# Kernel optimization log

Hardware: AMD Instinct MI355X
Metric: run time of the kernel (lower is better)

The kernel has to match this reference:

```python
import jax, jax.numpy as jnp
import numpy as np
from jax import lax

WINDOW_SIZE = 11
SIGMA = 1.5
MAX_VAL = 1.0
C1 = (0.01 * MAX_VAL) ** 2
C2 = (0.03 * MAX_VAL) ** 2
PAD = (WINDOW_SIZE - 1) // 2


def _gaussian_kernel2d(ksize: int, sigma: float) -> jnp.ndarray:
    x = jnp.arange(ksize, dtype=jnp.float32) - ksize // 2
    g = jnp.exp(-(x ** 2) / (2.0 * sigma ** 2))
    g = g / jnp.sum(g)
    return jnp.outer(g, g)  # [k, k]


def _filter2d(x: jnp.ndarray, kernel2d: jnp.ndarray) -> jnp.ndarray:
    # depthwise conv: x [B,C,H,W], kernel repeated per channel -> [C,1,k,k]
    c = x.shape[1]
    k = jnp.broadcast_to(kernel2d[None, None], (c, 1, WINDOW_SIZE, WINDOW_SIZE)).astype(x.dtype)
    return lax.conv_general_dilated(
        x, k,
        window_strides=(1, 1),
        padding=((PAD, PAD), (PAD, PAD)),
        dimension_numbers=("NCHW", "OIHW", "NCHW"),
        feature_group_count=c,
    )


def setup_inputs() -> dict:
    key = jax.random.key(0)
    k1, k2 = jax.random.split(key)
    img1 = jax.random.uniform(k1, (16, 3, 512, 512), dtype=jnp.float32)
    img2 = jax.random.uniform(k2, (16, 3, 512, 512), dtype=jnp.float32)
    return {"img1": img1, "img2": img2}


def reference(img1, img2):
    kernel = _gaussian_kernel2d(WINDOW_SIZE, SIGMA)
    mu1 = _filter2d(img1, kernel)
    mu2 = _filter2d(img2, kernel)
    mu1_sq = mu1 * mu1
    mu2_sq = mu2 * mu2
    mu1_mu2 = mu1 * mu2
    sigma1_sq = _filter2d(img1 * img1, kernel) - mu1_sq
    sigma2_sq = _filter2d(img2 * img2, kernel) - mu2_sq
    sigma12 = _filter2d(img1 * img2, kernel) - mu1_mu2
    ssim_map = ((2.0 * mu1_mu2 + C1) * (2.0 * sigma12 + C2)) / (
        (mu1_sq + mu2_sq + C1) * (sigma1_sq + sigma2_sq + C2)
    )
    loss = jnp.clip(1.0 - ssim_map, 0.0, 1.0) / 2.0
    return jnp.mean(loss)  # reduction='mean'
```

## Files before the change

kernel.cpp:

```cpp
#include <hip/hip_runtime.h>


#define BATCH  16
#define CHAN   3
#define H_     512
#define W_     512
#define HW     (H_ * W_)
#define CH_H   32
#define NSTEP  (CH_H + 10)
#define NPIX   ((long)BATCH*CHAN*H_*W_)

#define GW0 0.0010284f
#define GW1 0.0075988f
#define GW2 0.0360008f
#define GW3 0.1093554f
#define GW4 0.2130056f
#define GW5 0.2660117f

typedef float v2  __attribute__((ext_vector_type(2)));
typedef float v4f __attribute__((ext_vector_type(4)));

__device__ __forceinline__ float wg(int k) {
    return (k == 0 || k == 10) ? GW0
         : (k == 1 || k == 9)  ? GW1
         : (k == 2 || k == 8)  ? GW2
         : (k == 3 || k == 7)  ? GW3
         : (k == 4 || k == 6)  ? GW4 : GW5;
}

__device__ __forceinline__ v2 pfma(v2 a, v2 b, v2 c) {
#if __has_builtin(__builtin_elementwise_fma)
    return __builtin_elementwise_fma(a, b, c);
#else
    v2 r; r.x = fmaf(a.x, b.x, c.x); r.y = fmaf(a.y, b.y, c.y); return r;
#endif
}
__device__ __forceinline__ v2 psfma(float s, v2 b, v2 c) {
    v2 sv; sv.x = s; sv.y = s;
    return pfma(sv, b, c);
}

__device__ __forceinline__ float ssim_retire(float mu1, float mu2,
                                             float x11, float x22, float x12) {
    const float c1 = 1.0e-4f;
    const float c2 = 9.0e-4f;
    float mu1s = mu1 * mu1;
    float mu2s = mu2 * mu2;
    float m12  = mu1 * mu2;
    float num  = (2.0f * m12 + c1) * (2.0f * (x12 - m12) + c2);
    float den  = (mu1s + mu2s + c1) * ((x11 - mu1s) + (x22 - mu2s) + c2);
#if __has_builtin(__builtin_amdgcn_rcpf)
    float l = 1.0f - num * __builtin_amdgcn_rcpf(den);
#else
    float l = 1.0f - num / den;
#endif
    return fminf(fmaxf(l, 0.0f), 1.0f);
}

#define DECL(i) v2 PA##i = {0.f,0.f}, QA##i = {0.f,0.f}, PB##i = {0.f,0.f}, \
                   QB##i = {0.f,0.f}; float EA##i = 0.f, EB##i = 0.f
#define ACCI(i) do { const float wj_ = wg(10 - (i));             \
    PA##i = psfma(wj_, hmmA, PA##i);                             \
    QA##i = psfma(wj_, hssA, QA##i);                             \
    EA##i = fmaf(wj_, hm12A, EA##i);                             \
    PB##i = psfma(wj_, hmmB, PB##i);                             \
    QB##i = psfma(wj_, hssB, QB##i);                             \
    EB##i = fmaf(wj_, hm12B, EB##i); } while (0)
#define SHIFT(i, j) PA##i = PA##j; QA##i = QA##j; EA##i = EA##j; \
                    PB##i = PB##j; QB##i = QB##j; EB##i = EB##j

#define HT_A(ab_, k_) { v2 t = (ab_) * wg(k_); hmmA += t; \
    hssA = pfma(t, (ab_), hssA); hm12A = fmaf(t.x, (ab_).y, hm12A); }
#define HT_B(ab_, k_) { v2 t = (ab_) * wg(k_); hmmB += t; \
    hssB = pfma(t, (ab_), hssB); hm12B = fmaf(t.x, (ab_).y, hm12B); }

__global__ __launch_bounds__(256) void ssim_kernel(const float* __restrict__ img1,
                                                   const float* __restrict__ img2,
                                                   float* __restrict__ out) {
    __shared__ __align__(16) v2 sp[4][144];
    __shared__ float wsum[4];

    const int tid  = threadIdx.x;
    const int lane = tid & 63;
    const int wv   = tid >> 6;

    const int wid   = blockIdx.x * 4 + wv;
    const int plane = wid >> 6;
    const int rem   = wid & 63;
    const int strip = rem & 3;
    const int chunk = rem >> 2;
    const int y0 = chunk * CH_H;
    const int c0 = strip * 128;

    const int  cg   = c0 - 6 + 2 * lane;
    const bool cok  = (cg >= 0);
    const int  cix  = cok ? cg : 0;
    const float msk = cok ? 1.0f : 0.0f;
    const int  hg   = c0 + 122 + 2 * lane;
    const bool hok  = (lane < 6) && (hg + 1 < W_);
    const int  hix  = hok ? hg : 0;
    const float hmsk = hok ? 1.0f : 0.0f;

    const size_t pb = (size_t)plane * HW;
    const float* __restrict__ p1 = img1 + pb;
    const float* __restrict__ p2 = img2 + pb;

    v2* st = sp[wv];

    DECL(0); DECL(1); DECL(2); DECL(3); DECL(4); DECL(5);
    DECL(6); DECL(7); DECL(8); DECL(9); DECL(10);
    float lsum = 0.0f;

    v2 ma, mb, ha, hb;
    {
        int r = y0 - 5;
        bool rok = (unsigned)r < (unsigned)H_;
        size_t off = (size_t)(rok ? r : 0) * W_;
        float mm = rok ? msk : 0.0f, hm = rok ? hmsk : 0.0f;
        ma = *(const v2*)(p1 + off + cix) * mm;
        mb = *(const v2*)(p2 + off + cix) * mm;
        ha = *(const v2*)(p1 + off + hix) * hm;
        hb = *(const v2*)(p2 + off + hix) * hm;
    }

#pragma unroll 2
    for (int step = 0; step < NSTEP; ++step) {
        const int yy = step - 10;

        {
            v4f w; w.x = ma.x; w.y = mb.x; w.z = ma.y; w.w = mb.y;
            *(v4f*)&st[2 * lane] = w;
            if (lane < 6) {
                v4f wh; wh.x = ha.x; wh.y = hb.x; wh.z = ha.y; wh.w = hb.y;
                *(v4f*)&st[128 + 2 * lane] = wh;
            }
        }
        __asm__ __volatile__("" ::: "memory");

        {
            int r = y0 + step - 4;
            bool rok = (unsigned)r < (unsigned)H_;
            size_t off = (size_t)(rok ? r : 0) * W_;
            float mm = rok ? msk : 0.0f, hm = rok ? hmsk : 0.0f;
            ma = *(const v2*)(p1 + off + cix) * mm;
            mb = *(const v2*)(p2 + off + cix) * mm;
            ha = *(const v2*)(p1 + off + hix) * hm;
            hb = *(const v2*)(p2 + off + hix) * hm;
        }

        v2 m1  = st[2 * lane + 1];
        v4f r1 = *(const v4f*)&st[2 * lane + 2];
        v4f r2 = *(const v4f*)&st[2 * lane + 4];
        v4f r3 = *(const v4f*)&st[2 * lane + 6];
        v4f r4 = *(const v4f*)&st[2 * lane + 8];
        v4f r5 = *(const v4f*)&st[2 * lane + 10];
        v2 m12 = st[2 * lane + 12];
        v2 m2  = {r1.x, r1.y}, m3  = {r1.z, r1.w};
        v2 m4  = {r2.x, r2.y}, m5  = {r2.z, r2.w};
        v2 m6  = {r3.x, r3.y}, m7  = {r3.z, r3.w};
        v2 m8  = {r4.x, r4.y}, m9  = {r4.z, r4.w};
        v2 m10 = {r5.x, r5.y}, m11 = {r5.z, r5.w};

        v2 hmmA = m1 * wg(0);
        v2 hssA = hmmA * m1;
        float hm12A = hmmA.x * m1.y;
        HT_A(m2, 1); HT_A(m3, 2); HT_A(m4, 3); HT_A(m5, 4); HT_A(m6, 5);
        HT_A(m7, 6); HT_A(m8, 7); HT_A(m9, 8); HT_A(m10, 9); HT_A(m11, 10);
        v2 hmmB = m2 * wg(0);
        v2 hssB = hmmB * m2;
        float hm12B = hmmB.x * m2.y;
        HT_B(m3, 1); HT_B(m4, 2); HT_B(m5, 3); HT_B(m6, 4); HT_B(m7, 5);
        HT_B(m8, 6); HT_B(m9, 7); HT_B(m10, 8); HT_B(m11, 9); HT_B(m12, 10);
        __asm__ __volatile__("" ::: "memory");

        ACCI(0); ACCI(1); ACCI(2); ACCI(3); ACCI(4); ACCI(5);
        ACCI(6); ACCI(7); ACCI(8); ACCI(9); ACCI(10);

        if (yy >= 0) {
            lsum += ssim_retire(PA0.x, PA0.y, QA0.x, QA0.y, EA0);
            lsum += ssim_retire(PB0.x, PB0.y, QB0.x, QB0.y, EB0);
        }

        SHIFT(0, 1); SHIFT(1, 2); SHIFT(2, 3); SHIFT(3, 4); SHIFT(4, 5);
        SHIFT(5, 6); SHIFT(6, 7); SHIFT(7, 8); SHIFT(8, 9); SHIFT(9, 10);
        PA10 = (v2){0.f, 0.f}; QA10 = (v2){0.f, 0.f}; EA10 = 0.f;
        PB10 = (v2){0.f, 0.f}; QB10 = (v2){0.f, 0.f}; EB10 = 0.f;
    }

#pragma unroll
    for (int off = 32; off > 0; off >>= 1) lsum += __shfl_down(lsum, off);
    if (lane == 0) wsum[wv] = lsum;
    __syncthreads();
    if (tid == 0) {
        float bs = wsum[0] + wsum[1] + wsum[2] + wsum[3];
        atomicAdd(out, bs * (0.5f / (float)NPIX));
    }
}

extern "C" void kernel_launch(void* const* d_in, const int* in_sizes, int n_in,
                              void* d_out, int out_size, void* d_ws, size_t ws_size,
                              hipStream_t stream) {
    const float* img1 = (const float*)d_in[0];
    const float* img2 = (const float*)d_in[1];
    float* out = (float*)d_out;

    hipMemsetAsync(out, 0, sizeof(float), stream);

    ssim_kernel<<<dim3(4 * 16 * BATCH * CHAN / 4), 256, 0, stream>>>(img1, img2, out);
}
```

Measured before the change: 157.0 us.

## Split wave into two half-strips, double chunk height, trim vertical accumulator

Each 64-lane wavefront now covers two 64-column half-strips, one per 32-lane half, with separate shared staging, and row chunks grow from 32 to 64 rows. This shrinks the 10-row vertical halo overhead per output row. The vertical ring drops one register slot by seeding the newest slot directly from the horizontal sums, and blocks are one wave each with a direct atomic per wave. The trade-off is more horizontal halo columns per output (12 per 64 instead of 12 per 128), fewer blocks (1536 waves), and more atomics.

```diff
diff --git a/kernel.cpp b/kernel.cpp
--- a/kernel.cpp
+++ b/kernel.cpp
@@ -6,7 +6,7 @@
 #define H_     512
 #define W_     512
 #define HW     (H_ * W_)
-#define CH_H   32
+#define CH_H   64
 #define NSTEP  (CH_H + 10)
 #define NPIX   ((long)BATCH*CHAN*H_*W_)
 
@@ -74,30 +74,40 @@
 #define HT_B(ab_, k_) { v2 t = (ab_) * wg(k_); hmmB += t; \
     hssB = pfma(t, (ab_), hssB); hm12B = fmaf(t.x, (ab_).y, hm12B); }
 
-__global__ __launch_bounds__(256) void ssim_kernel(const float* __restrict__ img1,
-                                                   const float* __restrict__ img2,
-                                                   float* __restrict__ out) {
-    __shared__ __align__(16) v2 sp[4][144];
-    __shared__ float wsum[4];
+#define LOADROW(r_) do {                                           \
+    int rr_ = (r_);                                                \
+    bool rok_ = (unsigned)rr_ < (unsigned)H_;                      \
+    size_t off_ = ((size_t)(rok_ ? rr_ : 0) << 9);                 \
+    float mm_ = rok_ ? msk  : 0.0f;                                \
+    float hm_ = rok_ ? hmsk : 0.0f;                                \
+    ma = *(const v2*)(p1 + off_ + cix) * mm_;                      \
+    mb = *(const v2*)(p2 + off_ + cix) * mm_;                      \
+    ha = *(const v2*)(p1 + off_ + hix) * hm_;                      \
+    hb = *(const v2*)(p2 + off_ + hix) * hm_; } while (0)
 
-    const int tid  = threadIdx.x;
-    const int lane = tid & 63;
-    const int wv   = tid >> 6;
+__global__ __launch_bounds__(64) void ssim_kernel(const float* __restrict__ img1,
+                                                  const float* __restrict__ img2,
+                                                  float* __restrict__ out) {
+    __shared__ __align__(16) v2 sp[2][80];
 
-    const int wid   = blockIdx.x * 4 + wv;
-    const int plane = wid >> 6;
-    const int rem   = wid & 63;
-    const int strip = rem & 3;
+    const int lane = threadIdx.x & 63;
+    const int half = lane >> 5;
+    const int l    = lane & 31;
+
+    const int wid   = blockIdx.x;
+    const int plane = wid >> 5;
+    const int rem   = wid & 31;
+    const int t     = rem & 3;
     const int chunk = rem >> 2;
-    const int y0 = chunk * CH_H;
-    const int c0 = strip * 128;
+    const int y0  = chunk * CH_H;
+    const int c0h = t * 128 + half * 64;
 
-    const int  cg   = c0 - 6 + 2 * lane;
+    const int  cg   = c0h - 6 + 2 * l;
     const bool cok  = (cg >= 0);
     const int  cix  = cok ? cg : 0;
     const float msk = cok ? 1.0f : 0.0f;
-    const int  hg   = c0 + 122 + 2 * lane;
-    const bool hok  = (lane < 6) && (hg + 1 < W_);
+    const int  hg   = c0h + 58 + 2 * l;
+    const bool hok  = (l < 6) && (hg + 1 < W_);
     const int  hix  = hok ? hg : 0;
     const float hmsk = hok ? 1.0f : 0.0f;
 
@@ -105,23 +115,14 @@
     const float* __restrict__ p1 = img1 + pb;
     const float* __restrict__ p2 = img2 + pb;
 
-    v2* st = sp[wv];
+    v2* st = sp[half];
 
-    DECL(0); DECL(1); DECL(2); DECL(3); DECL(4); DECL(5);
-    DECL(6); DECL(7); DECL(8); DECL(9); DECL(10);
+    DECL(0); DECL(1); DECL(2); DECL(3); DECL(4);
+    DECL(5); DECL(6); DECL(7); DECL(8); DECL(9);
     float lsum = 0.0f;
 
     v2 ma, mb, ha, hb;
-    {
-        int r = y0 - 5;
-        bool rok = (unsigned)r < (unsigned)H_;
-        size_t off = (size_t)(rok ? r : 0) * W_;
-        float mm = rok ? msk : 0.0f, hm = rok ? hmsk : 0.0f;
-        ma = *(const v2*)(p1 + off + cix) * mm;
-        mb = *(const v2*)(p2 + off + cix) * mm;
-        ha = *(const v2*)(p1 + off + hix) * hm;
-        hb = *(const v2*)(p2 + off + hix) * hm;
-    }
+    LOADROW(y0 - 5);
 
 #pragma unroll 2
     for (int step = 0; step < NSTEP; ++step) {
@@ -129,32 +130,23 @@
 
         {
             v4f w; w.x = ma.x; w.y = mb.x; w.z = ma.y; w.w = mb.y;
-            *(v4f*)&st[2 * lane] = w;
-            if (lane < 6) {
+            *(v4f*)&st[2 * l] = w;
+            if (l < 6) {
                 v4f wh; wh.x = ha.x; wh.y = hb.x; wh.z = ha.y; wh.w = hb.y;
-                *(v4f*)&st[128 + 2 * lane] = wh;
+                *(v4f*)&st[64 + 2 * l] = wh;
             }
         }
         __asm__ __volatile__("" ::: "memory");
 
-        {
-            int r = y0 + step - 4;
-            bool rok = (unsigned)r < (unsigned)H_;
-            size_t off = (size_t)(rok ? r : 0) * W_;
-            float mm = rok ? msk : 0.0f, hm = rok ? hmsk : 0.0f;
-            ma = *(const v2*)(p1 + off + cix) * mm;
-            mb = *(const v2*)(p2 + off + cix) * mm;
-            ha = *(const v2*)(p1 + off + hix) * hm;
-            hb = *(const v2*)(p2 + off + hix) * hm;
-        }
+        LOADROW(y0 + step - 4);
 
-        v2 m1  = st[2 * lane + 1];
-        v4f r1 = *(const v4f*)&st[2 * lane + 2];
-        v4f r2 = *(const v4f*)&st[2 * lane + 4];
-        v4f r3 = *(const v4f*)&st[2 * lane + 6];
-        v4f r4 = *(const v4f*)&st[2 * lane + 8];
-        v4f r5 = *(const v4f*)&st[2 * lane + 10];
-        v2 m12 = st[2 * lane + 12];
+        v2 m1  = st[2 * l + 1];
+        v4f r1 = *(const v4f*)&st[2 * l + 2];
+        v4f r2 = *(const v4f*)&st[2 * l + 4];
+        v4f r3 = *(const v4f*)&st[2 * l + 6];
+        v4f r4 = *(const v4f*)&st[2 * l + 8];
+        v4f r5 = *(const v4f*)&st[2 * l + 10];
+        v2 m12 = st[2 * l + 12];
         v2 m2  = {r1.x, r1.y}, m3  = {r1.z, r1.w};
         v2 m4  = {r2.x, r2.y}, m5  = {r2.z, r2.w};
         v2 m6  = {r3.x, r3.y}, m7  = {r3.z, r3.w};
@@ -173,8 +165,8 @@
         HT_B(m8, 6); HT_B(m9, 7); HT_B(m10, 8); HT_B(m11, 9); HT_B(m12, 10);
         __asm__ __volatile__("" ::: "memory");
 
-        ACCI(0); ACCI(1); ACCI(2); ACCI(3); ACCI(4); ACCI(5);
-        ACCI(6); ACCI(7); ACCI(8); ACCI(9); ACCI(10);
+        ACCI(0); ACCI(1); ACCI(2); ACCI(3); ACCI(4);
+        ACCI(5); ACCI(6); ACCI(7); ACCI(8); ACCI(9);
 
         if (yy >= 0) {
             lsum += ssim_retire(PA0.x, PA0.y, QA0.x, QA0.y, EA0);
@@ -182,19 +174,14 @@
         }
 
         SHIFT(0, 1); SHIFT(1, 2); SHIFT(2, 3); SHIFT(3, 4); SHIFT(4, 5);
-        SHIFT(5, 6); SHIFT(6, 7); SHIFT(7, 8); SHIFT(8, 9); SHIFT(9, 10);
-        PA10 = (v2){0.f, 0.f}; QA10 = (v2){0.f, 0.f}; EA10 = 0.f;
-        PB10 = (v2){0.f, 0.f}; QB10 = (v2){0.f, 0.f}; EB10 = 0.f;
+        SHIFT(5, 6); SHIFT(6, 7); SHIFT(7, 8); SHIFT(8, 9);
+        PA9 = hmmA * wg(0); QA9 = hssA * wg(0); EA9 = hm12A * wg(0);
+        PB9 = hmmB * wg(0); QB9 = hssB * wg(0); EB9 = hm12B * wg(0);
     }
 
 #pragma unroll
     for (int off = 32; off > 0; off >>= 1) lsum += __shfl_down(lsum, off);
-    if (lane == 0) wsum[wv] = lsum;
-    __syncthreads();
-    if (tid == 0) {
-        float bs = wsum[0] + wsum[1] + wsum[2] + wsum[3];
-        atomicAdd(out, bs * (0.5f / (float)NPIX));
-    }
+    if (lane == 0) atomicAdd(out, lsum * (0.5f / (float)NPIX));
 }
 
 extern "C" void kernel_launch(void* const* d_in, const int* in_sizes, int n_in,
@@ -206,5 +193,5 @@
 
     hipMemsetAsync(out, 0, sizeof(float), stream);
 
-    ssim_kernel<<<dim3(4 * 16 * BATCH * CHAN / 4), 256, 0, stream>>>(img1, img2, out);
+    ssim_kernel<<<dim3(4 * 8 * BATCH * CHAN), 64, 0, stream>>>(img1, img2, out);
 }
```

After: 165.7 us. 5.5% more time.
